# Performance work log

Measured on AMD Instinct MI355X. Metric: run time of the kernel, lower is better.

Reference implementation:

```python
import jax, jax.numpy as jnp
import numpy as np
import math

S, B, D = 2048, 2, 1024
H = 16
DH = D // H
WIN = 256
DIL = 1


def setup_inputs() -> dict:
    key = jax.random.key(0)
    ks = jax.random.split(key, 10)
    std = 1.0 / math.sqrt(D)
    return {
        "x": jax.random.normal(ks[0], (S, B, D), jnp.float32),
        "beta": jax.random.normal(ks[1], (H,), jnp.float32) * 0.02,
        "Wq": jax.random.normal(ks[2], (D, D), jnp.float32) * std,
        "bq": jnp.zeros((D,), jnp.float32),
        "Wk": jax.random.normal(ks[3], (D, D), jnp.float32) * std,
        "bk": jnp.zeros((D,), jnp.float32),
        "Wv": jax.random.normal(ks[4], (D, D), jnp.float32) * std,
        "bv": jnp.zeros((D,), jnp.float32),
        "Wo": jax.random.normal(ks[5], (D, D), jnp.float32) * std,
        "bo": jnp.zeros((D,), jnp.float32),
    }


def _split_heads(t):
    # (S, B, D) -> (B*H, S, DH), matching rearrange 's b (h d) -> (b h) s d'
    return t.reshape(S, B, H, DH).transpose(1, 2, 0, 3).reshape(B * H, S, DH)


def reference(x, beta, Wq, bq, Wk, bk, Wv, bv, Wo, bo):
    q = _split_heads(x @ Wq + bq)
    k = _split_heads(x @ Wk + bk)
    v = _split_heads(x @ Wv + bv)

    # per-head learnable temperature: q / (sqrt(d_head) * exp(beta))
    beta_exp = jnp.tile(jnp.exp(beta), B)  # (B*H,), head index = z % H
    q = q / (jnp.sqrt(jnp.asarray(DH, x.dtype)) * beta_exp)[:, None, None]

    # causal dilated windowed mask
    idx = jnp.arange(S)
    diff = idx[:, None] - idx[None, :]
    allowed = (diff >= 0) & (diff <= DIL * (WIN - 1)) & (diff % DIL == 0)
    mask = jnp.where(allowed, jnp.asarray(0.0, x.dtype), jnp.asarray(-jnp.inf, x.dtype))

    scores = jnp.einsum('zqd,zkd->zqk', q, k) + mask[None]
    # attention sink: extra zero-logit column absorbing probability mass
    scores = jnp.concatenate([scores, jnp.zeros((B * H, S, 1), scores.dtype)], axis=-1)
    attn = jax.nn.softmax(scores, axis=-1)[..., :-1]

    out = jnp.einsum('zqk,zkd->zqd', attn, v)
    # (B*H, S, DH) -> (S, B, D)
    out = out.reshape(B, H, S, DH).transpose(2, 0, 1, 3).reshape(S, B, D)
    return out @ Wo + bo
```

## Files before the change

kernel.cpp:

```cpp
#include <hip/hip_runtime.h>
#include <math.h>

#define S_LEN  2048
#define BATCH  2
#define DM     1024
#define NHEAD  16
#define DHEAD  64
#define WIN    256
#define MROWS  4096

#define KP   72
#define PPAD 68

typedef __attribute__((ext_vector_type(8))) short bf16x8;
typedef __attribute__((ext_vector_type(4))) float f32x4;

__device__ __forceinline__ unsigned short f2b(float f) {
    unsigned int u = __float_as_uint(f);
    return (unsigned short)((u + 0x7fffu + ((u >> 16) & 1u)) >> 16);
}
__device__ __forceinline__ void gld16(const void* g, void* l) {
    __builtin_amdgcn_global_load_lds(
        (const __attribute__((address_space(1))) void*)g,
        (__attribute__((address_space(3))) void*)l, 16, 0, 0);
}
__device__ __forceinline__ bf16x8 pack8(float4 a, float4 b) {
    bf16x8 r;
    r[0] = (short)f2b(a.x); r[1] = (short)f2b(a.y);
    r[2] = (short)f2b(a.z); r[3] = (short)f2b(a.w);
    r[4] = (short)f2b(b.x); r[5] = (short)f2b(b.y);
    r[6] = (short)f2b(b.z); r[7] = (short)f2b(b.w);
    return r;
}

__global__ __launch_bounds__(256)
void cvtx(const float* __restrict__ x, unsigned short* __restrict__ xb)
{
    const int i = (blockIdx.x * 256 + threadIdx.x) * 4;
    float4 f = *(const float4*)(x + i);
    ushort4 o; o.x = f2b(f.x); o.y = f2b(f.y); o.z = f2b(f.z); o.w = f2b(f.w);
    *(ushort4*)(xb + i) = o;
}

__global__ __launch_bounds__(256)
void twcvt4(const float* __restrict__ W0, const float* __restrict__ W1,
            const float* __restrict__ W2, const float* __restrict__ W3,
            unsigned short* __restrict__ T0, unsigned short* __restrict__ T1,
            unsigned short* __restrict__ T2, unsigned short* __restrict__ T3)
{
    const int zz = blockIdx.z;
    const float* W = (zz == 0) ? W0 : (zz == 1) ? W1 : (zz == 2) ? W2 : W3;
    unsigned short* WT = (zz == 0) ? T0 : (zz == 1) ? T1 : (zz == 2) ? T2 : T3;

    __shared__ float t32[32][33];
    const int bx = blockIdx.x * 32;
    const int by = blockIdx.y * 32;
    const int c  = threadIdx.x & 31;
    const int r0 = threadIdx.x >> 5;
#pragma unroll
    for (int p = 0; p < 4; ++p)
        t32[r0 + 8 * p][c] = W[(size_t)(by + r0 + 8 * p) * DM + bx + c];
    __syncthreads();
#pragma unroll
    for (int p = 0; p < 4; ++p)
        WT[(size_t)(bx + r0 + 8 * p) * DM + by + c] = f2b(t32[c][r0 + 8 * p]);
}

__global__ __launch_bounds__(256)
void vtrans(const unsigned short* __restrict__ v, unsigned short* __restrict__ vt)
{
    __shared__ unsigned short T[64 * 72];
    const int z  = blockIdx.y;
    const int s0 = blockIdx.x * 64;
    const int t  = threadIdx.x;
#pragma unroll
    for (int i = 0; i < 2; ++i) {
        const int id = t + 256 * i;
        const int r  = id >> 3;
        const int c8 = (id & 7) * 8;
        *(bf16x8*)&T[r * 72 + c8] =
            *(const bf16x8*)(v + ((size_t)z * S_LEN + s0 + r) * DHEAD + c8);
    }
    __syncthreads();
    const int dh = t & 63, sg = t >> 6;
#pragma unroll
    for (int i = 0; i < 2; ++i) {
        const int sb = (sg + 4 * i) * 8;
        bf16x8 o;
#pragma unroll
        for (int e = 0; e < 8; ++e) o[e] = T[(sb + e) * 72 + dh];
        *(bf16x8*)(vt + ((size_t)z * DHEAD + dh) * S_LEN + s0 + sb) = o;
    }
}

__global__ __launch_bounds__(256)
void gemm_mfma(const unsigned short* __restrict__ A,
               const unsigned short* __restrict__ BT,
               const float* __restrict__ b0,
               const float* __restrict__ b1,
               const float* __restrict__ b2,
               const float* __restrict__ beta,
               float* __restrict__ Cf,
               unsigned short* __restrict__ Cb,
               int mode)
{
    __shared__ unsigned short As[128 * 32];
    __shared__ unsigned short Bs[128 * 32];

    const int t  = threadIdx.x;
    const int wv = t >> 6, ln = t & 63;
    const int rowBase = blockIdx.y * 128;
    const int colBase = blockIdx.x * 128;

    const int m16 = ln & 15, g = ln >> 4;
    const int wr = wv >> 1, wc = wv & 1;
    const int swz = m16 & 3;

    const int lr = ln >> 2;
    const int lq = (ln & 3) ^ (lr & 3);
    const unsigned short* ga = A  + (size_t)(rowBase + wv * 16 + lr) * DM + lq * 8;
    const unsigned short* gb = BT + (size_t)(colBase + wv * 16 + lr) * DM + lq * 8;
    unsigned short* la0 = As + wv * 512;
    unsigned short* la1 = la0 + 2048;
    unsigned short* lb0 = Bs + wv * 512;
    unsigned short* lb1 = lb0 + 2048;

    f32x4 acc[4][4];
#pragma unroll
    for (int u = 0; u < 4; ++u)
#pragma unroll
        for (int v = 0; v < 4; ++v)
            acc[u][v] = (f32x4){0.f, 0.f, 0.f, 0.f};

    for (int kb = 0; kb < DM; kb += 32) {
        gld16(ga + kb, la0);
        gld16(ga + (size_t)64 * DM + kb, la1);
        gld16(gb + kb, lb0);
        gld16(gb + (size_t)64 * DM + kb, lb1);
        __syncthreads();

        bf16x8 af[4], bfr[4];
#pragma unroll
        for (int u = 0; u < 4; ++u)
            af[u] = *(const bf16x8*)&As[(wr * 64 + u * 16 + m16) * 32 + ((g ^ swz) * 8)];
#pragma unroll
        for (int v = 0; v < 4; ++v)
            bfr[v] = *(const bf16x8*)&Bs[(wc * 64 + v * 16 + m16) * 32 + ((g ^ swz) * 8)];
#pragma unroll
        for (int u = 0; u < 4; ++u)
#pragma unroll
            for (int v = 0; v < 4; ++v)
                acc[u][v] = __builtin_amdgcn_mfma_f32_16x16x32_bf16(
                    af[u], bfr[v], acc[u][v], 0, 0, 0);
        __syncthreads();
    }

    const int q4 = g * 4;
    if (mode == 0) {
#pragma unroll
        for (int v = 0; v < 4; ++v) {
            const int col = colBase + wc * 64 + v * 16 + m16;
            const float bi = b0[col];
#pragma unroll
            for (int u = 0; u < 4; ++u)
#pragma unroll
                for (int r = 0; r < 4; ++r) {
                    const int row = rowBase + wr * 64 + u * 16 + q4 + r;
                    Cf[(size_t)row * DM + col] = acc[u][v][r] + bi;
                }
        }
    } else {
#pragma unroll
        for (int v = 0; v < 4; ++v) {
            const int col = colBase + wc * 64 + v * 16 + m16;
            const int sec = col >> 10;
            const int h   = (col >> 6) & (NHEAD - 1);
            const int dh  = col & 63;
            const float bi = (sec == 0 ? b0 : sec == 1 ? b1 : b2)[col & (DM - 1)];
            const float sc = (sec == 0) ? 0.125f * __expf(-beta[h]) : 1.0f;
            unsigned short* base = Cb + (size_t)sec * MROWS * DM;
#pragma unroll
            for (int u = 0; u < 4; ++u)
#pragma unroll
                for (int r = 0; r < 4; ++r) {
                    const int row = rowBase + wr * 64 + u * 16 + q4 + r;
                    const int s = row >> 1, bb = row & 1;
                    const int z = bb * NHEAD + h;
                    base[((size_t)z * S_LEN + s) * DHEAD + dh] =
                        f2b((acc[u][v][r] + bi) * sc);
                }
        }
    }
}

__global__ __launch_bounds__(256, 4)
void attn_mfma(const unsigned short* __restrict__ q,
               const unsigned short* __restrict__ k,
               const unsigned short* __restrict__ vt,
               unsigned short* __restrict__ ao)
{
    __shared__ unsigned short Ks[64 * KP];
    __shared__ unsigned short Vs[64 * KP];
    __shared__ float Ps[64][PPAD];

    const int t   = threadIdx.x;
    const int wv  = t >> 6, ln = t & 63;
    const int m16 = ln & 15, g = ln >> 4;
    const int z   = blockIdx.y;
    const int q0  = blockIdx.x * 64;
    const size_t zbase = (size_t)z * S_LEN * DHEAD;

    const unsigned short* qrow = q + zbase + (size_t)(q0 + wv * 16 + m16) * DHEAD;
    bf16x8 qf0 = *(const bf16x8*)(qrow + g * 8);
    bf16x8 qf1 = *(const bf16x8*)(qrow + 32 + g * 8);

    f32x4 oacc[4];
#pragma unroll
    for (int v4 = 0; v4 < 4; ++v4) oacc[v4] = (f32x4){0.f, 0.f, 0.f, 0.f};
    float mr[4], lr[4];
#pragma unroll
    for (int r = 0; r < 4; ++r) { mr[r] = 0.f; lr[r] = 1.f; }

    for (int c = 0; c < 5; ++c) {
        const int kb = q0 - 256 + c * 64;
        if (kb < 0) continue;
        __syncthreads();

#pragma unroll
        for (int i = 0; i < 2; ++i) {
            const int id  = t + 256 * i;
            const int row = id >> 3;
            const int co  = (id & 7) * 8;
            *(bf16x8*)&Ks[row * KP + co] =
                *(const bf16x8*)(k + zbase + (size_t)(kb + row) * DHEAD + co);
            *(bf16x8*)&Vs[row * KP + co] =
                *(const bf16x8*)(vt + ((size_t)z * DHEAD + row) * S_LEN + kb + co);
        }
        __syncthreads();

        f32x4 sacc[4];
#pragma unroll
        for (int v4 = 0; v4 < 4; ++v4) {
            sacc[v4] = (f32x4){0.f, 0.f, 0.f, 0.f};
            bf16x8 kf0 = *(const bf16x8*)&Ks[(v4 * 16 + m16) * KP + g * 8];
            sacc[v4] = __builtin_amdgcn_mfma_f32_16x16x32_bf16(qf0, kf0, sacc[v4], 0, 0, 0);
            bf16x8 kf1 = *(const bf16x8*)&Ks[(v4 * 16 + m16) * KP + 32 + g * 8];
            sacc[v4] = __builtin_amdgcn_mfma_f32_16x16x32_bf16(qf1, kf1, sacc[v4], 0, 0, 0);
        }

        const bool mhi = (c == 4), mlo = (c == 0);
#pragma unroll
        for (int r = 0; r < 4; ++r) {
            const int ig = q0 + wv * 16 + g * 4 + r;
            float sv[4];
            float smax = -1e30f;
#pragma unroll
            for (int v4 = 0; v4 < 4; ++v4) {
                const int jg = kb + v4 * 16 + m16;
                float x = sacc[v4][r];
                const bool valid = (!mhi || jg <= ig) && (!mlo || jg >= ig - (WIN - 1));
                x = valid ? x : -1e30f;
                sv[v4] = x;
                smax = fmaxf(smax, x);
            }
#pragma unroll
            for (int off = 1; off < 16; off <<= 1)
                smax = fmaxf(smax, __shfl_xor(smax, off, 64));
            const float mnew  = fmaxf(mr[r], smax);
            const float alpha = __expf(mr[r] - mnew);
            float rsum = 0.f;
#pragma unroll
            for (int v4 = 0; v4 < 4; ++v4) {
                const float pp = __expf(sv[v4] - mnew);
                Ps[wv * 16 + g * 4 + r][v4 * 16 + m16] = pp;
                rsum += pp;
            }
#pragma unroll
            for (int off = 1; off < 16; off <<= 1)
                rsum += __shfl_xor(rsum, off, 64);
            lr[r] = lr[r] * alpha + rsum;
            mr[r] = mnew;
#pragma unroll
            for (int v4 = 0; v4 < 4; ++v4) oacc[v4][r] *= alpha;
        }
        __syncthreads();

        const float* prow = &Ps[wv * 16 + m16][0];
        bf16x8 pf0 = pack8(*(const float4*)(prow + g * 8),
                           *(const float4*)(prow + g * 8 + 4));
        bf16x8 pf1 = pack8(*(const float4*)(prow + 32 + g * 8),
                           *(const float4*)(prow + 32 + g * 8 + 4));
#pragma unroll
        for (int v4 = 0; v4 < 4; ++v4) {
            bf16x8 vf0 = *(const bf16x8*)&Vs[(v4 * 16 + m16) * KP + g * 8];
            oacc[v4] = __builtin_amdgcn_mfma_f32_16x16x32_bf16(pf0, vf0, oacc[v4], 0, 0, 0);
            bf16x8 vf1 = *(const bf16x8*)&Vs[(v4 * 16 + m16) * KP + 32 + g * 8];
            oacc[v4] = __builtin_amdgcn_mfma_f32_16x16x32_bf16(pf1, vf1, oacc[v4], 0, 0, 0);
        }
    }

    const int bb = z >> 4, h = z & 15;
#pragma unroll
    for (int r = 0; r < 4; ++r) {
        const int ig  = q0 + wv * 16 + g * 4 + r;
        const float inv = 1.f / lr[r];
#pragma unroll
        for (int v4 = 0; v4 < 4; ++v4)
            ao[(size_t)(ig * BATCH + bb) * DM + h * DHEAD + v4 * 16 + m16] =
                f2b(oacc[v4][r] * inv);
    }
}

extern "C" void kernel_launch(void* const* d_in, const int* in_sizes, int n_in,
                              void* d_out, int out_size, void* d_ws, size_t ws_size,
                              hipStream_t stream)
{
    const float* x    = (const float*)d_in[0];
    const float* beta = (const float*)d_in[1];
    const float* Wq   = (const float*)d_in[2];
    const float* bq   = (const float*)d_in[3];
    const float* Wk   = (const float*)d_in[4];
    const float* bk   = (const float*)d_in[5];
    const float* Wv   = (const float*)d_in[6];
    const float* bv   = (const float*)d_in[7];
    const float* Wo   = (const float*)d_in[8];
    const float* bo   = (const float*)d_in[9];
    float* out = (float*)d_out;

    unsigned short* w = (unsigned short*)d_ws;
    const size_t seg = (size_t)MROWS * DM;
    unsigned short* qb  = w;
    unsigned short* kb  = w + seg;
    unsigned short* vb  = w + 2 * seg;
    unsigned short* ab  = w + 3 * seg;
    unsigned short* xb  = w + 4 * seg;
    unsigned short* wtq = w + 5 * seg;
    unsigned short* wtk = wtq + (size_t)DM * DM;
    unsigned short* wtv = wtk + (size_t)DM * DM;
    unsigned short* wto = wtv + (size_t)DM * DM;
    unsigned short* vtb = xb;

    cvtx<<<4096, 256, 0, stream>>>(x, xb);
    twcvt4<<<dim3(32, 32, 4), 256, 0, stream>>>(Wq, Wk, Wv, Wo, wtq, wtk, wtv, wto);

    gemm_mfma<<<dim3(3072 / 128, MROWS / 128), 256, 0, stream>>>(
        xb, wtq, bq, bk, bv, beta, nullptr, qb, 1);

    vtrans<<<dim3(S_LEN / 64, BATCH * NHEAD), 256, 0, stream>>>(vb, vtb);

    attn_mfma<<<dim3(S_LEN / 64, BATCH * NHEAD), 256, 0, stream>>>(qb, kb, vtb, ab);

    gemm_mfma<<<dim3(DM / 128, MROWS / 128), 256, 0, stream>>>(
        ab, wto, bo, nullptr, nullptr, beta, out, nullptr, 0);
}
```

Measured before the change: 198.2 us.

## Fuse V transpose into QKV GEMM epilogue and change LDS swizzle pattern

The QKV projection GEMM epilogue now writes the V section directly in transposed (z, dh, s) layout using paired 2-element stores, so the separate vtrans kernel launch and its extra read/write of V are removed. The LDS XOR swizzle in the GEMM is changed to key on pairs of rows instead of single rows, to alter the bank conflict pattern for the MFMA fragment loads. The transposed V stores are strided across S and only 4 bytes wide, so that part of the epilogue may be less coalesced than before.

```diff
diff --git a/kernel.cpp b/kernel.cpp
--- a/kernel.cpp
+++ b/kernel.cpp
@@ -64,33 +64,6 @@
 #pragma unroll
     for (int p = 0; p < 4; ++p)
         WT[(size_t)(bx + r0 + 8 * p) * DM + by + c] = f2b(t32[c][r0 + 8 * p]);
-}
-
-__global__ __launch_bounds__(256)
-void vtrans(const unsigned short* __restrict__ v, unsigned short* __restrict__ vt)
-{
-    __shared__ unsigned short T[64 * 72];
-    const int z  = blockIdx.y;
-    const int s0 = blockIdx.x * 64;
-    const int t  = threadIdx.x;
-#pragma unroll
-    for (int i = 0; i < 2; ++i) {
-        const int id = t + 256 * i;
-        const int r  = id >> 3;
-        const int c8 = (id & 7) * 8;
-        *(bf16x8*)&T[r * 72 + c8] =
-            *(const bf16x8*)(v + ((size_t)z * S_LEN + s0 + r) * DHEAD + c8);
-    }
-    __syncthreads();
-    const int dh = t & 63, sg = t >> 6;
-#pragma unroll
-    for (int i = 0; i < 2; ++i) {
-        const int sb = (sg + 4 * i) * 8;
-        bf16x8 o;
-#pragma unroll
-        for (int e = 0; e < 8; ++e) o[e] = T[(sb + e) * 72 + dh];
-        *(bf16x8*)(vt + ((size_t)z * DHEAD + dh) * S_LEN + s0 + sb) = o;
-    }
 }
 
 __global__ __launch_bounds__(256)
@@ -114,10 +87,10 @@
 
     const int m16 = ln & 15, g = ln >> 4;
     const int wr = wv >> 1, wc = wv & 1;
-    const int swz = m16 & 3;
+    const int swz = (m16 >> 1) & 3;
 
     const int lr = ln >> 2;
-    const int lq = (ln & 3) ^ (lr & 3);
+    const int lq = (ln & 3) ^ ((lr >> 1) & 3);
     const unsigned short* ga = A  + (size_t)(rowBase + wv * 16 + lr) * DM + lq * 8;
     const unsigned short* gb = BT + (size_t)(colBase + wv * 16 + lr) * DM + lq * 8;
     unsigned short* la0 = As + wv * 512;
@@ -170,25 +143,48 @@
                 }
         }
     } else {
-#pragma unroll
-        for (int v = 0; v < 4; ++v) {
-            const int col = colBase + wc * 64 + v * 16 + m16;
-            const int sec = col >> 10;
-            const int h   = (col >> 6) & (NHEAD - 1);
-            const int dh  = col & 63;
-            const float bi = (sec == 0 ? b0 : sec == 1 ? b1 : b2)[col & (DM - 1)];
-            const float sc = (sec == 0) ? 0.125f * __expf(-beta[h]) : 1.0f;
-            unsigned short* base = Cb + (size_t)sec * MROWS * DM;
-#pragma unroll
-            for (int u = 0; u < 4; ++u)
-#pragma unroll
-                for (int r = 0; r < 4; ++r) {
-                    const int row = rowBase + wr * 64 + u * 16 + q4 + r;
-                    const int s = row >> 1, bb = row & 1;
-                    const int z = bb * NHEAD + h;
-                    base[((size_t)z * S_LEN + s) * DHEAD + dh] =
-                        f2b((acc[u][v][r] + bi) * sc);
+        const int sec = colBase >> 10;
+        if (sec < 2) {
+#pragma unroll
+            for (int v = 0; v < 4; ++v) {
+                const int col = colBase + wc * 64 + v * 16 + m16;
+                const int h   = (col >> 6) & (NHEAD - 1);
+                const int dh  = col & 63;
+                const float bi = (sec == 0 ? b0 : b1)[col & (DM - 1)];
+                const float sc = (sec == 0) ? 0.125f * __expf(-beta[h]) : 1.0f;
+                unsigned short* base = Cb + (size_t)sec * MROWS * DM;
+#pragma unroll
+                for (int u = 0; u < 4; ++u)
+#pragma unroll
+                    for (int r = 0; r < 4; ++r) {
+                        const int row = rowBase + wr * 64 + u * 16 + q4 + r;
+                        const int s = row >> 1, bb = row & 1;
+                        const int z = bb * NHEAD + h;
+                        base[((size_t)z * S_LEN + s) * DHEAD + dh] =
+                            f2b((acc[u][v][r] + bi) * sc);
+                    }
+            }
+        } else {
+            unsigned short* vtb = Cb + (size_t)2 * MROWS * DM;
+#pragma unroll
+            for (int v = 0; v < 4; ++v) {
+                const int col = colBase + wc * 64 + v * 16 + m16;
+                const int h   = (col >> 6) & (NHEAD - 1);
+                const int dh  = col & 63;
+                const float bi = b2[col & (DM - 1)];
+#pragma unroll
+                for (int u = 0; u < 4; ++u) {
+                    const int row0 = rowBase + wr * 64 + u * 16 + q4;
+                    const int s0   = row0 >> 1;
+                    ushort2 p0, p1;
+                    p0.x = f2b(acc[u][v][0] + bi);
+                    p0.y = f2b(acc[u][v][2] + bi);
+                    p1.x = f2b(acc[u][v][1] + bi);
+                    p1.y = f2b(acc[u][v][3] + bi);
+                    *(ushort2*)(vtb + ((size_t)(h * DHEAD + dh) * S_LEN + s0)) = p0;
+                    *(ushort2*)(vtb + ((size_t)((NHEAD + h) * DHEAD + dh) * S_LEN + s0)) = p1;
                 }
+            }
         }
     }
 }
@@ -331,14 +327,13 @@
     const size_t seg = (size_t)MROWS * DM;
     unsigned short* qb  = w;
     unsigned short* kb  = w + seg;
-    unsigned short* vb  = w + 2 * seg;
+    unsigned short* vtb = w + 2 * seg;
     unsigned short* ab  = w + 3 * seg;
     unsigned short* xb  = w + 4 * seg;
     unsigned short* wtq = w + 5 * seg;
     unsigned short* wtk = wtq + (size_t)DM * DM;
     unsigned short* wtv = wtk + (size_t)DM * DM;
     unsigned short* wto = wtv + (size_t)DM * DM;
-    unsigned short* vtb = xb;
 
     cvtx<<<4096, 256, 0, stream>>>(x, xb);
     twcvt4<<<dim3(32, 32, 4), 256, 0, stream>>>(Wq, Wk, Wv, Wo, wtq, wtk, wtv, wto);
@@ -346,8 +341,6 @@
     gemm_mfma<<<dim3(3072 / 128, MROWS / 128), 256, 0, stream>>>(
         xb, wtq, bq, bk, bv, beta, nullptr, qb, 1);
 
-    vtrans<<<dim3(S_LEN / 64, BATCH * NHEAD), 256, 0, stream>>>(vb, vtb);
-
     attn_mfma<<<dim3(S_LEN / 64, BATCH * NHEAD), 256, 0, stream>>>(qb, kb, vtb, ab);
 
     gemm_mfma<<<dim3(DM / 128, MROWS / 128), 256, 0, stream>>>(
```

Result: faster. 192.9 us (-2.7%).
